# Kernel optimization log

Measured on AMD Instinct MI355X. Metric: run time of the kernel, lower is better.

The kernel has to match this reference:

```python
import jax, jax.numpy as jnp
import numpy as np
import math

L = 12      # n_layer (alternating adaptive True/False)
H = 8       # n_head
C = 256     # n_embd
DH = C // H # head dim = 32
BS = 828    # block_size
T = 827     # seq len after dropping last token
VOCAB = 16384
CAM = 30
IMG = 256


def get_sinusoid(n_position, d_hid):
    pos = np.arange(n_position)[:, None].astype(np.float64)
    hid = np.arange(d_hid)[None, :]
    angle = pos / np.power(10000.0, 2.0 * (hid // 2) / d_hid)
    table = np.zeros_like(angle)
    table[:, 0::2] = np.sin(angle[:, 0::2])
    table[:, 1::2] = np.cos(angle[:, 1::2])
    return jnp.asarray(table[None], jnp.float32)  # [1, n_position, d_hid]


def layer_norm(x, w, b):
    m = x.mean(-1, keepdims=True)
    v = ((x - m) ** 2).mean(-1, keepdims=True)
    return (x - m) * jax.lax.rsqrt(v + 1e-5) * w + b


def setup_inputs() -> dict:
    key = jax.random.key(0)
    ks = iter(jax.random.split(key, 64))
    nrm = lambda shape, s=1.0: jax.random.normal(next(ks), shape, jnp.float32) * s
    B = 4
    inp = {
        'dc_emb': nrm((B, 572, C)),
        'z_emb': nrm((B, 256, C)),
        'p1': nrm((B, CAM)),
        'p2': nrm((B, CAM)),
        'p3': nrm((B, CAM)),
        'frame_emb': nrm((1, 256, C), 0.02),
        'camera_emb': nrm((1, 30, C), 0.02),
        'time_emb': get_sinusoid(BS, C),
        'loc_W1': nrm((2 * CAM, CAM), 0.02), 'loc_b1': jnp.zeros((2 * CAM,)),
        'loc_W2': nrm((IMG * IMG, 2 * CAM), 0.02), 'loc_b2': jnp.zeros((IMG * IMG,)),
        'ln1_w': jnp.ones((L, C)), 'ln1_b': jnp.zeros((L, C)),
        'Wq': nrm((L, C, C), 0.02), 'bq': jnp.zeros((L, C)),
        'Wk': nrm((L, C, C), 0.02), 'bk': jnp.zeros((L, C)),
        'Wv': nrm((L, C, C), 0.02), 'bv': jnp.zeros((L, C)),
        'Wo': nrm((L, C, C), 0.02), 'bo': jnp.zeros((L, C)),
        'ln2_w': jnp.ones((L, C)), 'ln2_b': jnp.zeros((L, C)),
        'W1': nrm((L, 4 * C, C), 0.02), 'b1': jnp.zeros((L, 4 * C)),
        'W2': nrm((L, C, 4 * C), 0.02), 'b2': jnp.zeros((L, C)),
        'lnf_w': jnp.ones((C,)), 'lnf_b': jnp.zeros((C,)),
        'head_W': nrm((VOCAB, C), 0.02),
    }
    return inp


def _forward(dc_emb, z_emb, p1, p2, p3, frame_emb, camera_emb, time_emb,
             loc_W1, loc_b1, loc_W2, loc_b2,
             ln1_w, ln1_b, Wq, bq, Wk, bk, Wv, bv, Wo, bo,
             ln2_w, ln2_b, W1, b1, W2, b2, lnf_w, lnf_b, head_W):
    B = dc_emb.shape[0]
    scale = 1.0 / math.sqrt(DH)

    # AdaptiveAttention bias h: [B, 1, BS, BS] with three 256x256 learned blocks
    def locality(p):
        z = jax.nn.gelu(p @ loc_W1.T + loc_b1, approximate=False)
        z = z @ loc_W2.T + loc_b2
        return z.reshape(B, IMG, IMG)

    h = jnp.zeros((B, 1, BS, BS), dc_emb.dtype)
    h = h.at[:, 0, 285:541, 0:256].set(locality(p1))
    h = h.at[:, 0, 571:827, 0:256].set(locality(p2))
    h = h.at[:, 0, 571:827, 286:542].set(locality(p3))
    h = h[:, :, :T, :T]

    # token + role + time embeddings
    tok = jnp.concatenate([dc_emb, z_emb], axis=1)[:, :-1, :]  # [B, T, C]
    role = jnp.concatenate([frame_emb, camera_emb, frame_emb, camera_emb, frame_emb], axis=1)[:, :T, :]
    x = tok + role + time_emb[:, :T, :]

    causal = jnp.tril(jnp.ones((T, T), bool))  # [T, T]

    for i in range(L):
        adaptive = (i % 2 == 0)
        xn = layer_norm(x, ln1_w[i], ln1_b[i])
        q = (xn @ Wq[i].T + bq[i]).reshape(B, T, H, DH)
        k = (xn @ Wk[i].T + bk[i]).reshape(B, T, H, DH)
        v = (xn @ Wv[i].T + bv[i]).reshape(B, T, H, DH)
        att = jnp.einsum('bqhd,bkhd->bhqk', q, k) * scale
        if adaptive:
            att = att + h
        att = jnp.where(causal, att, -jnp.inf)
        att = jax.nn.softmax(att, axis=-1)
        y = jnp.einsum('bhqk,bkhd->bqhd', att, v).reshape(B, T, C)
        x = x + y @ Wo[i].T + bo[i]
        xn2 = layer_norm(x, ln2_w[i], ln2_b[i])
        x = x + jax.nn.gelu(xn2 @ W1[i].T + b1[i], approximate=False) @ W2[i].T + b2[i]

    x = layer_norm(x, lnf_w, lnf_b)
    logits = x @ head_W.T  # [B, T, VOCAB]
    return logits


def reference(dc_emb, z_emb, p1, p2, p3, frame_emb, camera_emb, time_emb,
              loc_W1, loc_b1, loc_W2, loc_b2,
              ln1_w, ln1_b, Wq, bq, Wk, bk, Wv, bv, Wo, bo,
              ln2_w, ln2_b, W1, b1, W2, b2, lnf_w, lnf_b, head_W):
    return _forward(dc_emb, z_emb, p1, p2, p3, frame_emb, camera_emb, time_emb,
                    loc_W1, loc_b1, loc_W2, loc_b2,
                    ln1_w, ln1_b, Wq, bq, Wk, bk, Wv, bv, Wo, bo,
                    ln2_w, ln2_b, W1, b1, W2, b2, lnf_w, lnf_b, head_W)
```

## Files before the change

kernel.cpp:

```cpp
#include <hip/hip_runtime.h>
#include <hip/hip_bf16.h>
#include <math.h>

#define T_LEN 827
#define M_ROWS 3308
#define NLAYER 12

typedef __attribute__((ext_vector_type(4))) float f32x4;
typedef __attribute__((ext_vector_type(8))) short bf16x8;

__device__ __forceinline__ float gelu_f(float x) {
    return 0.5f * x * (1.0f + erff(x * 0.70710678118654752440f));
}

__device__ __forceinline__ short f2bf_s(float x) {
    __hip_bfloat16 h = __float2bfloat16(x);
    return *reinterpret_cast<short*>(&h);
}

__global__ void cvt_kernel(const float* __restrict__ in, __hip_bfloat16* __restrict__ out, int n4) {
    int i = blockIdx.x * blockDim.x + threadIdx.x;
    if (i >= n4) return;
    float4 v = reinterpret_cast<const float4*>(in)[i];
    out[4*i+0] = __float2bfloat16(v.x);
    out[4*i+1] = __float2bfloat16(v.y);
    out[4*i+2] = __float2bfloat16(v.z);
    out[4*i+3] = __float2bfloat16(v.w);
}

__global__ void prep_wqkv_kernel(const float* __restrict__ Wq, const float* __restrict__ Wk,
                                 const float* __restrict__ Wv, __hip_bfloat16* __restrict__ out) {
    int i = blockIdx.x * 256 + threadIdx.x;
    if (i >= 12*768*64) return;
    int el = i * 4;
    int layer = el / (768*256);
    int rem = el % (768*256);
    int row = rem >> 8, col = rem & 255;
    const float* src;
    float sc = 1.f;
    if (row < 256)      { src = Wq + ((size_t)layer*256 + row)*256 + col; sc = 0.17677669529663687f; }
    else if (row < 512) { src = Wk + ((size_t)layer*256 + (row-256))*256 + col; }
    else                { src = Wv + ((size_t)layer*256 + (row-512))*256 + col; }
    float4 v = *reinterpret_cast<const float4*>(src);
    out[el+0] = __float2bfloat16(v.x * sc);
    out[el+1] = __float2bfloat16(v.y * sc);
    out[el+2] = __float2bfloat16(v.z * sc);
    out[el+3] = __float2bfloat16(v.w * sc);
}

__global__ void prep_bqkv_kernel(const float* __restrict__ bq, const float* __restrict__ bk,
                                 const float* __restrict__ bv, float* __restrict__ out) {
    int i = blockIdx.x * 256 + threadIdx.x;
    if (i >= 12*768) return;
    int layer = i / 768, row = i % 768;
    float v;
    if (row < 256)      v = bq[layer*256 + row] * 0.17677669529663687f;
    else if (row < 512) v = bk[layer*256 + (row-256)];
    else                v = bv[layer*256 + (row-512)];
    out[i] = v;
}

__global__ void zero_kernel(float* __restrict__ p, int n) {
    for (int i = blockIdx.x * blockDim.x + threadIdx.x; i < n; i += gridDim.x * blockDim.x)
        p[i] = 0.f;
}

__global__ void loc_z1_kernel(const float* __restrict__ p1, const float* __restrict__ p2,
                              const float* __restrict__ p3, const float* __restrict__ W1,
                              const float* __restrict__ b1, float* __restrict__ z1) {
    for (int i = threadIdx.x; i < 720; i += 256) {
        int pi = i / 240, rem = i % 240, b = rem / 60, j = rem % 60;
        const float* p = (pi == 0) ? p1 : ((pi == 1) ? p2 : p3);
        float acc = b1[j];
        #pragma unroll
        for (int c = 0; c < 30; ++c) acc += p[b*30 + c] * W1[j*30 + c];
        z1[i] = gelu_f(acc);
    }
}

__global__ void h_fill_kernel(const float* __restrict__ z1, const float* __restrict__ W2,
                              const float* __restrict__ b2, float* __restrict__ h) {
    __shared__ float z[720];
    int tid = threadIdx.x;
    for (int i = tid; i < 720; i += 256) z[i] = z1[i];
    __syncthreads();
    int j = blockIdx.x * 256 + tid;
    float w[60];
    #pragma unroll
    for (int c = 0; c < 60; ++c) w[c] = W2[(size_t)j*60 + c];
    float bj = b2[j];
    int r = j >> 8, cc = j & 255;
    const int br[3] = {285, 571, 571};
    const int bc[3] = {0, 0, 286};
    #pragma unroll
    for (int pi = 0; pi < 3; ++pi) {
        for (int b = 0; b < 4; ++b) {
            float acc = bj;
            #pragma unroll
            for (int c = 0; c < 60; ++c) acc += z[pi*240 + b*60 + c] * w[c];
            h[(size_t)b*T_LEN*T_LEN + (size_t)(br[pi] + r)*T_LEN + bc[pi] + cc] = acc;
        }
    }
}

__global__ void init_x_kernel(const float* __restrict__ dc, const float* __restrict__ z,
                              const float* __restrict__ frame, const float* __restrict__ cam,
                              const float* __restrict__ timeE, float* __restrict__ x) {
    int idx = blockIdx.x * 256 + threadIdx.x;
    int m = idx >> 8, c = idx & 255;
    int b = m / T_LEN, t = m % T_LEN;
    float tok = (t < 572) ? dc[((size_t)b*572 + t)*256 + c]
                          : z[((size_t)b*256 + (t - 572))*256 + c];
    float role;
    if      (t < 256) role = frame[t*256 + c];
    else if (t < 286) role = cam[(t-256)*256 + c];
    else if (t < 542) role = frame[(t-286)*256 + c];
    else if (t < 572) role = cam[(t-542)*256 + c];
    else              role = frame[(t-572)*256 + c];
    x[idx] = tok + role + timeE[t*256 + c];
}

__global__ __launch_bounds__(256) void ln_kernel(const float* __restrict__ x,
                                                 const float* __restrict__ w,
                                                 const float* __restrict__ b,
                                                 __hip_bfloat16* __restrict__ out) {
    int row = blockIdx.x, tid = threadIdx.x;
    float v = x[(size_t)row*256 + tid];
    float s = v;
    #pragma unroll
    for (int off = 32; off; off >>= 1) s += __shfl_down(s, off);
    __shared__ float red[4];
    if ((tid & 63) == 0) red[tid >> 6] = s;
    __syncthreads();
    float mean = (red[0] + red[1] + red[2] + red[3]) * (1.f/256.f);
    float d = v - mean;
    float s2 = d * d;
    #pragma unroll
    for (int off = 32; off; off >>= 1) s2 += __shfl_down(s2, off);
    __shared__ float red2[4];
    if ((tid & 63) == 0) red2[tid >> 6] = s2;
    __syncthreads();
    float var = (red2[0] + red2[1] + red2[2] + red2[3]) * (1.f/256.f);
    float rs = rsqrtf(var + 1e-5f);
    out[(size_t)row*256 + tid] = __float2bfloat16(d * rs * w[tid] + b[tid]);
}

template<int ACT, bool OUTBF16, bool RESID>
__global__ __launch_bounds__(256) void gemm_kernel(const __hip_bfloat16* __restrict__ A,
                                                   const __hip_bfloat16* __restrict__ W,
                                                   const float* __restrict__ bias,
                                                   const float* __restrict__ resid,
                                                   void* __restrict__ out,
                                                   int M, int N, int K, float alpha) {
    __shared__ __hip_bfloat16 As[64][40];
    __shared__ __hip_bfloat16 Bs[64][40];
    const int tid = threadIdx.x;
    const int m0 = blockIdx.x * 64;
    const int n0 = blockIdx.y * 64;
    const int wid = tid >> 6, lane = tid & 63;
    const int wm = wid >> 1, wn = wid & 1;
    const int fr = lane & 15, fq = lane >> 4;
    const int srow = tid >> 2;
    const int scol = (tid & 3) * 8;

    f32x4 acc[2][2];
    #pragma unroll
    for (int mi = 0; mi < 2; ++mi)
        #pragma unroll
        for (int ni = 0; ni < 2; ++ni)
            acc[mi][ni] = (f32x4){0.f, 0.f, 0.f, 0.f};

    for (int k0 = 0; k0 < K; k0 += 32) {
        int gm = m0 + srow;
        uint4 av = make_uint4(0u, 0u, 0u, 0u);
        if (gm < M) av = *reinterpret_cast<const uint4*>(A + (size_t)gm*K + k0 + scol);
        *reinterpret_cast<uint4*>(&As[srow][scol]) = av;
        int gn = n0 + srow;
        uint4 bv = *reinterpret_cast<const uint4*>(W + (size_t)gn*K + k0 + scol);
        *reinterpret_cast<uint4*>(&Bs[srow][scol]) = bv;
        __syncthreads();
        bf16x8 af[2], bfr[2];
        af[0] = *reinterpret_cast<const bf16x8*>(&As[wm*32 + fr][fq*8]);
        af[1] = *reinterpret_cast<const bf16x8*>(&As[wm*32 + 16 + fr][fq*8]);
        bfr[0] = *reinterpret_cast<const bf16x8*>(&Bs[wn*32 + fr][fq*8]);
        bfr[1] = *reinterpret_cast<const bf16x8*>(&Bs[wn*32 + 16 + fr][fq*8]);
        #pragma unroll
        for (int mi = 0; mi < 2; ++mi)
            #pragma unroll
            for (int ni = 0; ni < 2; ++ni)
                acc[mi][ni] = __builtin_amdgcn_mfma_f32_16x16x32_bf16(af[mi], bfr[ni], acc[mi][ni], 0, 0, 0);
        __syncthreads();
    }

    #pragma unroll
    for (int mi = 0; mi < 2; ++mi) {
        #pragma unroll
        for (int ni = 0; ni < 2; ++ni) {
            int n = n0 + wn*32 + ni*16 + fr;
            float bv = bias ? bias[n] : 0.f;
            #pragma unroll
            for (int r = 0; r < 4; ++r) {
                int m = m0 + wm*32 + mi*16 + fq*4 + r;
                if (m >= M) continue;
                float v = (acc[mi][ni][r] + bv) * alpha;
                if (RESID) v += resid[(size_t)m*N + n];
                if (ACT == 1) v = gelu_f(v);
                if (OUTBF16) ((__hip_bfloat16*)out)[(size_t)m*N + n] = __float2bfloat16(v);
                else         ((float*)out)[(size_t)m*N + n] = v;
            }
        }
    }
}

template<int ADAPT>
__global__ __launch_bounds__(256) void attn_mfma_kernel(const __hip_bfloat16* __restrict__ qkv,
                                                        const float* __restrict__ hbuf,
                                                        __hip_bfloat16* __restrict__ y) {
    const int qi = blockIdx.x, hh = blockIdx.y, b = blockIdx.z;
    const int tid = threadIdx.x;
    const int w = tid >> 6, lane = tid & 63;
    const int c = lane & 15, g = lane >> 4;
    const int q0 = qi * 64;
    const int qw0 = q0 + w * 16;

    __shared__ short Ks[64][40];
    __shared__ short Vt[32][72];
    __shared__ short Pw[4][16][72];

    int qrow = qw0 + c; if (qrow > T_LEN-1) qrow = T_LEN-1;
    bf16x8 aq = *reinterpret_cast<const bf16x8*>(qkv + ((size_t)b*T_LEN + qrow)*768 + hh*32 + g*8);

    float m_r[4] = {-INFINITY, -INFINITY, -INFINITY, -INFINITY};
    float l_r[4] = {0.f, 0.f, 0.f, 0.f};
    f32x4 acc[2];
    acc[0] = (f32x4){0.f,0.f,0.f,0.f};
    acc[1] = (f32x4){0.f,0.f,0.f,0.f};

    const int nk = min(q0 + 64, T_LEN);
    const int srow = tid >> 2;
    const int scol8 = (tid & 3) * 8;

    for (int kb = 0; kb < nk; kb += 64) {
        int krow = kb + srow; if (krow > T_LEN-1) krow = T_LEN-1;
        const __hip_bfloat16* kvbase = qkv + ((size_t)b*T_LEN + krow)*768 + hh*32 + scol8;
        bf16x8 kv8 = *reinterpret_cast<const bf16x8*>(kvbase + 256);
        *reinterpret_cast<bf16x8*>(&Ks[srow][scol8]) = kv8;
        bf16x8 vv8 = *reinterpret_cast<const bf16x8*>(kvbase + 512);
        #pragma unroll
        for (int jj = 0; jj < 8; ++jj) Vt[scol8 + jj][srow] = vv8[jj];
        __syncthreads();

        f32x4 sc4[4];
        #pragma unroll
        for (int j = 0; j < 4; ++j) {
            bf16x8 bk = *reinterpret_cast<const bf16x8*>(&Ks[j*16 + c][g*8]);
            sc4[j] = __builtin_amdgcn_mfma_f32_16x16x32_bf16(aq, bk, (f32x4){0.f,0.f,0.f,0.f}, 0, 0, 0);
        }

        float sv[4][4];
        #pragma unroll
        for (int j = 0; j < 4; ++j) {
            int kk = kb + j*16 + c;
            #pragma unroll
            for (int r = 0; r < 4; ++r) {
                int qq = qw0 + g*4 + r;
                bool valid = (qq < T_LEN) && (kk <= qq);
                float s = sc4[j][r];
                if (ADAPT) s += valid ? hbuf[((size_t)b*T_LEN + qq)*T_LEN + kk] : 0.f;
                sv[j][r] = valid ? s : -INFINITY;
            }
        }

        float rm[4], rs[4], sf[4];
        #pragma unroll
        for (int r = 0; r < 4; ++r) {
            float m = fmaxf(fmaxf(sv[0][r], sv[1][r]), fmaxf(sv[2][r], sv[3][r]));
            #pragma unroll
            for (int msk = 1; msk <= 8; msk <<= 1) m = fmaxf(m, __shfl_xor(m, msk));
            float mn = fmaxf(m_r[r], m);
            sf[r] = __expf(m_r[r] - mn);
            m_r[r] = mn;
        }
        float p[4][4];
        #pragma unroll
        for (int r = 0; r < 4; ++r) {
            float su = 0.f;
            #pragma unroll
            for (int j = 0; j < 4; ++j) {
                float e = __expf(sv[j][r] - m_r[r]);
                p[j][r] = e;
                su += e;
            }
            #pragma unroll
            for (int msk = 1; msk <= 8; msk <<= 1) su += __shfl_xor(su, msk);
            rs[r] = su;
            l_r[r] = l_r[r] * sf[r] + rs[r];
            acc[0][r] *= sf[r];
            acc[1][r] *= sf[r];
        }

        #pragma unroll
        for (int j = 0; j < 4; ++j)
            #pragma unroll
            for (int r = 0; r < 4; ++r)
                Pw[w][g*4 + r][j*16 + c] = f2bf_s(p[j][r]);

        #pragma unroll
        for (int kc = 0; kc < 2; ++kc) {
            bf16x8 ap = *reinterpret_cast<const bf16x8*>(&Pw[w][c][kc*32 + g*8]);
            #pragma unroll
            for (int dt = 0; dt < 2; ++dt) {
                bf16x8 bv = *reinterpret_cast<const bf16x8*>(&Vt[dt*16 + c][kc*32 + g*8]);
                acc[dt] = __builtin_amdgcn_mfma_f32_16x16x32_bf16(ap, bv, acc[dt], 0, 0, 0);
            }
        }
        __syncthreads();
    }

    #pragma unroll
    for (int r = 0; r < 4; ++r) {
        int qq = qw0 + g*4 + r;
        if (qq >= T_LEN) continue;
        float inv = 1.f / l_r[r];
        #pragma unroll
        for (int dt = 0; dt < 2; ++dt)
            y[((size_t)b*T_LEN + qq)*256 + hh*32 + dt*16 + c] = __float2bfloat16(acc[dt][r] * inv);
    }
}

extern "C" void kernel_launch(void* const* d_in, const int* in_sizes, int n_in,
                              void* d_out, int out_size, void* d_ws, size_t ws_size,
                              hipStream_t stream) {
    const float* dc    = (const float*)d_in[0];
    const float* zemb  = (const float*)d_in[1];
    const float* p1    = (const float*)d_in[2];
    const float* p2    = (const float*)d_in[3];
    const float* p3    = (const float*)d_in[4];
    const float* frame = (const float*)d_in[5];
    const float* cam   = (const float*)d_in[6];
    const float* timeE = (const float*)d_in[7];
    const float* locW1 = (const float*)d_in[8];
    const float* locb1 = (const float*)d_in[9];
    const float* locW2 = (const float*)d_in[10];
    const float* locb2 = (const float*)d_in[11];
    const float* ln1w  = (const float*)d_in[12];
    const float* ln1b  = (const float*)d_in[13];
    const float* Wq    = (const float*)d_in[14];
    const float* bq    = (const float*)d_in[15];
    const float* Wk    = (const float*)d_in[16];
    const float* bk    = (const float*)d_in[17];
    const float* Wv    = (const float*)d_in[18];
    const float* bv    = (const float*)d_in[19];
    const float* Wo    = (const float*)d_in[20];
    const float* bo    = (const float*)d_in[21];
    const float* ln2w  = (const float*)d_in[22];
    const float* ln2b  = (const float*)d_in[23];
    const float* W1p   = (const float*)d_in[24];
    const float* b1p   = (const float*)d_in[25];
    const float* W2p   = (const float*)d_in[26];
    const float* b2p   = (const float*)d_in[27];
    const float* lnfw  = (const float*)d_in[28];
    const float* lnfb  = (const float*)d_in[29];
    const float* headW = (const float*)d_in[30];

    char* wsb = (char*)d_ws;
    size_t off = 0;
    auto alloc = [&](size_t bytes) -> char* {
        char* p = wsb + off;
        off += (bytes + 255) & ~(size_t)255;
        return p;
    };
    __hip_bfloat16* wqkv_bf = (__hip_bfloat16*)alloc(12ull*768*256*2);
    float*          bqkv    = (float*)alloc(12ull*768*4);
    __hip_bfloat16* wo_bf = (__hip_bfloat16*)alloc(12ull*65536*2);
    __hip_bfloat16* w1_bf = (__hip_bfloat16*)alloc(12ull*262144*2);
    __hip_bfloat16* w2_bf = (__hip_bfloat16*)alloc(12ull*262144*2);
    __hip_bfloat16* wh_bf = (__hip_bfloat16*)alloc(16384ull*256*2);
    float* hbuf = (float*)alloc(4ull*T_LEN*T_LEN*4);
    float* x    = (float*)alloc((size_t)M_ROWS*256*4);
    __hip_bfloat16* xn   = (__hip_bfloat16*)alloc((size_t)M_ROWS*256*2);
    __hip_bfloat16* qkvb = (__hip_bfloat16*)alloc((size_t)M_ROWS*768*2);
    __hip_bfloat16* yb   = (__hip_bfloat16*)alloc((size_t)M_ROWS*256*2);
    __hip_bfloat16* mid  = (__hip_bfloat16*)alloc((size_t)M_ROWS*1024*2);
    float* z1   = (float*)alloc(720*4);

    prep_wqkv_kernel<<<(12*768*64 + 255)/256, 256, 0, stream>>>(Wq, Wk, Wv, wqkv_bf);
    prep_bqkv_kernel<<<36, 256, 0, stream>>>(bq, bk, bv, bqkv);
    cvt_kernel<<<768, 256, 0, stream>>>(Wo, wo_bf, 196608);
    cvt_kernel<<<3072, 256, 0, stream>>>(W1p, w1_bf, 786432);
    cvt_kernel<<<3072, 256, 0, stream>>>(W2p, w2_bf, 786432);
    cvt_kernel<<<4096, 256, 0, stream>>>(headW, wh_bf, 1048576);

    loc_z1_kernel<<<1, 256, 0, stream>>>(p1, p2, p3, locW1, locb1, z1);
    zero_kernel<<<2048, 256, 0, stream>>>(hbuf, 4*T_LEN*T_LEN);
    h_fill_kernel<<<256, 256, 0, stream>>>(z1, locW2, locb2, hbuf);

    init_x_kernel<<<M_ROWS, 256, 0, stream>>>(dc, zemb, frame, cam, timeE, x);

    dim3 g256((M_ROWS + 63)/64, 256/64);
    dim3 g768((M_ROWS + 63)/64, 768/64);
    dim3 g1024((M_ROWS + 63)/64, 1024/64);
    dim3 gattn(13, 8, 4);

    for (int i = 0; i < NLAYER; ++i) {
        ln_kernel<<<M_ROWS, 256, 0, stream>>>(x, ln1w + i*256, ln1b + i*256, xn);
        gemm_kernel<0,true,false><<<g768, 256, 0, stream>>>(xn, wqkv_bf + (size_t)i*768*256, bqkv + i*768, nullptr, qkvb, M_ROWS, 768, 256, 1.f);
        if (i % 2 == 0) attn_mfma_kernel<1><<<gattn, 256, 0, stream>>>(qkvb, hbuf, yb);
        else            attn_mfma_kernel<0><<<gattn, 256, 0, stream>>>(qkvb, hbuf, yb);
        gemm_kernel<0,false,true><<<g256, 256, 0, stream>>>(yb, wo_bf + (size_t)i*65536, bo + i*256, x, x, M_ROWS, 256, 256, 1.f);
        ln_kernel<<<M_ROWS, 256, 0, stream>>>(x, ln2w + i*256, ln2b + i*256, xn);
        gemm_kernel<1,true,false><<<g1024, 256, 0, stream>>>(xn, w1_bf + (size_t)i*262144, b1p + i*1024, nullptr, mid, M_ROWS, 1024, 256, 1.f);
        gemm_kernel<0,false,true><<<g256, 256, 0, stream>>>(mid, w2_bf + (size_t)i*262144, b2p + i*256, x, x, M_ROWS, 256, 1024, 1.f);
    }

    ln_kernel<<<M_ROWS, 256, 0, stream>>>(x, lnfw, lnfb, xn);
    gemm_kernel<0,false,false><<<dim3(52, 256), 256, 0, stream>>>(xn, wh_bf, nullptr, nullptr, (float*)d_out, M_ROWS, 16384, 256, 1.f);
}
```

Before: 1.173 ms.

## Fuse layernorms into GEMMs, fuse MLP, and double-buffer attention K/V

Replaces the generic K-looped GEMM with a K=256 single-shot kernel that optionally applies layernorm on the A-operand load. It fuses LN2+FC1+GELU+FC2+residual (and the final LN) into one MLP kernel that keeps the hidden activations in shared memory. The attention kernel double-buffers K/V tiles with register prefetch and drops one barrier per iteration. This removes the separate LN launches and the 1024-wide intermediate round-trip through global memory. In exchange, the MLP kernel launches only 104 blocks and reads weights directly from global memory, which may leave the GPU underoccupied.

```diff
diff --git a/kernel.cpp b/kernel.cpp
--- a/kernel.cpp
+++ b/kernel.cpp
@@ -120,49 +120,68 @@
     x[idx] = tok + role + timeE[t*256 + c];
 }
 
-__global__ __launch_bounds__(256) void ln_kernel(const float* __restrict__ x,
-                                                 const float* __restrict__ w,
-                                                 const float* __restrict__ b,
-                                                 __hip_bfloat16* __restrict__ out) {
-    int row = blockIdx.x, tid = threadIdx.x;
-    float v = x[(size_t)row*256 + tid];
-    float s = v;
-    #pragma unroll
-    for (int off = 32; off; off >>= 1) s += __shfl_down(s, off);
-    __shared__ float red[4];
-    if ((tid & 63) == 0) red[tid >> 6] = s;
+template<bool LN, bool RESID, bool OUTBF16>
+__global__ __launch_bounds__(256) void gemm_k256(
+    const float* __restrict__ xsrc, const float* __restrict__ lnw, const float* __restrict__ lnb,
+    const __hip_bfloat16* __restrict__ Abf,
+    const __hip_bfloat16* __restrict__ W, const float* __restrict__ bias,
+    const float* __restrict__ resid, void* __restrict__ out, int M, int N)
+{
+    __shared__ __hip_bfloat16 As[64][264];
+    __shared__ __hip_bfloat16 Bs[64][264];
+    __shared__ float redS[4][64], redQ[4][64];
+    const int tid = threadIdx.x;
+    const int m0 = blockIdx.x * 64, n0 = blockIdx.y * 64;
+    const int r = tid >> 2, sg = tid & 3;
+
+    {
+        const __hip_bfloat16* bsrc = W + (size_t)(n0 + r) * 256 + sg * 8;
+        #pragma unroll
+        for (int j = 0; j < 8; ++j)
+            *reinterpret_cast<uint4*>(&Bs[r][sg*8 + j*32]) =
+                *reinterpret_cast<const uint4*>(bsrc + j*32);
+    }
+    int gr = m0 + r; if (gr > M-1) gr = M-1;
+    if constexpr (LN) {
+        const float* src = xsrc + (size_t)gr * 256;
+        float s = 0.f, q = 0.f;
+        #pragma unroll
+        for (int j = 0; j < 8; ++j) {
+            int k = sg*8 + j*32;
+            float4 a = *reinterpret_cast<const float4*>(src + k);
+            float4 c4 = *reinterpret_cast<const float4*>(src + k + 4);
+            s += a.x + a.y + a.z + a.w + c4.x + c4.y + c4.z + c4.w;
+            q += a.x*a.x + a.y*a.y + a.z*a.z + a.w*a.w
+               + c4.x*c4.x + c4.y*c4.y + c4.z*c4.z + c4.w*c4.w;
+        }
+        redS[sg][r] = s; redQ[sg][r] = q;
+        __syncthreads();
+        float mean = (redS[0][r] + redS[1][r] + redS[2][r] + redS[3][r]) * (1.f/256.f);
+        float msq  = (redQ[0][r] + redQ[1][r] + redQ[2][r] + redQ[3][r]) * (1.f/256.f);
+        float rstd = rsqrtf(msq - mean*mean + 1e-5f);
+        #pragma unroll
+        for (int j = 0; j < 8; ++j) {
+            int k = sg*8 + j*32;
+            float4 a = *reinterpret_cast<const float4*>(src + k);
+            float4 c4 = *reinterpret_cast<const float4*>(src + k + 4);
+            float v[8] = {a.x, a.y, a.z, a.w, c4.x, c4.y, c4.z, c4.w};
+            bf16x8 pk;
+            #pragma unroll
+            for (int e = 0; e < 8; ++e)
+                pk[e] = f2bf_s((v[e] - mean) * rstd * lnw[k+e] + lnb[k+e]);
+            *reinterpret_cast<bf16x8*>(&As[r][k]) = pk;
+        }
+    } else {
+        const __hip_bfloat16* asrc = Abf + (size_t)gr * 256 + sg * 8;
+        #pragma unroll
+        for (int j = 0; j < 8; ++j)
+            *reinterpret_cast<uint4*>(&As[r][sg*8 + j*32]) =
+                *reinterpret_cast<const uint4*>(asrc + j*32);
+    }
     __syncthreads();
-    float mean = (red[0] + red[1] + red[2] + red[3]) * (1.f/256.f);
-    float d = v - mean;
-    float s2 = d * d;
-    #pragma unroll
-    for (int off = 32; off; off >>= 1) s2 += __shfl_down(s2, off);
-    __shared__ float red2[4];
-    if ((tid & 63) == 0) red2[tid >> 6] = s2;
-    __syncthreads();
-    float var = (red2[0] + red2[1] + red2[2] + red2[3]) * (1.f/256.f);
-    float rs = rsqrtf(var + 1e-5f);
-    out[(size_t)row*256 + tid] = __float2bfloat16(d * rs * w[tid] + b[tid]);
-}
-
-template<int ACT, bool OUTBF16, bool RESID>
-__global__ __launch_bounds__(256) void gemm_kernel(const __hip_bfloat16* __restrict__ A,
-                                                   const __hip_bfloat16* __restrict__ W,
-                                                   const float* __restrict__ bias,
-                                                   const float* __restrict__ resid,
-                                                   void* __restrict__ out,
-                                                   int M, int N, int K, float alpha) {
-    __shared__ __hip_bfloat16 As[64][40];
-    __shared__ __hip_bfloat16 Bs[64][40];
-    const int tid = threadIdx.x;
-    const int m0 = blockIdx.x * 64;
-    const int n0 = blockIdx.y * 64;
+
     const int wid = tid >> 6, lane = tid & 63;
-    const int wm = wid >> 1, wn = wid & 1;
-    const int fr = lane & 15, fq = lane >> 4;
-    const int srow = tid >> 2;
-    const int scol = (tid & 3) * 8;
-
+    const int wm = wid >> 1, wn = wid & 1, c = lane & 15, g = lane >> 4;
     f32x4 acc[2][2];
     #pragma unroll
     for (int mi = 0; mi < 2; ++mi)
@@ -170,44 +189,170 @@
         for (int ni = 0; ni < 2; ++ni)
             acc[mi][ni] = (f32x4){0.f, 0.f, 0.f, 0.f};
 
-    for (int k0 = 0; k0 < K; k0 += 32) {
-        int gm = m0 + srow;
-        uint4 av = make_uint4(0u, 0u, 0u, 0u);
-        if (gm < M) av = *reinterpret_cast<const uint4*>(A + (size_t)gm*K + k0 + scol);
-        *reinterpret_cast<uint4*>(&As[srow][scol]) = av;
-        int gn = n0 + srow;
-        uint4 bv = *reinterpret_cast<const uint4*>(W + (size_t)gn*K + k0 + scol);
-        *reinterpret_cast<uint4*>(&Bs[srow][scol]) = bv;
-        __syncthreads();
-        bf16x8 af[2], bfr[2];
-        af[0] = *reinterpret_cast<const bf16x8*>(&As[wm*32 + fr][fq*8]);
-        af[1] = *reinterpret_cast<const bf16x8*>(&As[wm*32 + 16 + fr][fq*8]);
-        bfr[0] = *reinterpret_cast<const bf16x8*>(&Bs[wn*32 + fr][fq*8]);
-        bfr[1] = *reinterpret_cast<const bf16x8*>(&Bs[wn*32 + 16 + fr][fq*8]);
-        #pragma unroll
-        for (int mi = 0; mi < 2; ++mi)
-            #pragma unroll
-            for (int ni = 0; ni < 2; ++ni)
-                acc[mi][ni] = __builtin_amdgcn_mfma_f32_16x16x32_bf16(af[mi], bfr[ni], acc[mi][ni], 0, 0, 0);
-        __syncthreads();
+    #pragma unroll
+    for (int kj = 0; kj < 8; ++kj) {
+        bf16x8 a0 = *reinterpret_cast<const bf16x8*>(&As[wm*32 + c][kj*32 + g*8]);
+        bf16x8 a1 = *reinterpret_cast<const bf16x8*>(&As[wm*32 + 16 + c][kj*32 + g*8]);
+        bf16x8 b0 = *reinterpret_cast<const bf16x8*>(&Bs[wn*32 + c][kj*32 + g*8]);
+        bf16x8 b1v = *reinterpret_cast<const bf16x8*>(&Bs[wn*32 + 16 + c][kj*32 + g*8]);
+        acc[0][0] = __builtin_amdgcn_mfma_f32_16x16x32_bf16(a0, b0, acc[0][0], 0, 0, 0);
+        acc[0][1] = __builtin_amdgcn_mfma_f32_16x16x32_bf16(a0, b1v, acc[0][1], 0, 0, 0);
+        acc[1][0] = __builtin_amdgcn_mfma_f32_16x16x32_bf16(a1, b0, acc[1][0], 0, 0, 0);
+        acc[1][1] = __builtin_amdgcn_mfma_f32_16x16x32_bf16(a1, b1v, acc[1][1], 0, 0, 0);
     }
 
     #pragma unroll
     for (int mi = 0; mi < 2; ++mi) {
         #pragma unroll
         for (int ni = 0; ni < 2; ++ni) {
-            int n = n0 + wn*32 + ni*16 + fr;
-            float bv = bias ? bias[n] : 0.f;
-            #pragma unroll
-            for (int r = 0; r < 4; ++r) {
-                int m = m0 + wm*32 + mi*16 + fq*4 + r;
+            int n = n0 + wn*32 + ni*16 + c;
+            float bb = bias ? bias[n] : 0.f;
+            #pragma unroll
+            for (int rg = 0; rg < 4; ++rg) {
+                int m = m0 + wm*32 + mi*16 + g*4 + rg;
                 if (m >= M) continue;
-                float v = (acc[mi][ni][r] + bv) * alpha;
+                float v = acc[mi][ni][rg] + bb;
                 if (RESID) v += resid[(size_t)m*N + n];
-                if (ACT == 1) v = gelu_f(v);
                 if (OUTBF16) ((__hip_bfloat16*)out)[(size_t)m*N + n] = __float2bfloat16(v);
                 else         ((float*)out)[(size_t)m*N + n] = v;
             }
+        }
+    }
+}
+
+template<bool FINAL>
+__global__ __launch_bounds__(512) void mlp_fused(
+    float* __restrict__ x,
+    const float* __restrict__ ln2w, const float* __restrict__ ln2b,
+    const __hip_bfloat16* __restrict__ W1, const float* __restrict__ b1,
+    const __hip_bfloat16* __restrict__ W2, const float* __restrict__ b2,
+    const float* __restrict__ lnfw, const float* __restrict__ lnfb,
+    __hip_bfloat16* __restrict__ xn)
+{
+    __shared__ __hip_bfloat16 As[32][264];
+    __shared__ __hip_bfloat16 Ms[32][1044];
+    const int tid = threadIdx.x;
+    const int m0 = blockIdx.x * 32;
+    const int w = tid >> 6, lane = tid & 63, c = lane & 15, g = lane >> 4;
+
+    {
+        int r = tid >> 4, p = tid & 15;
+        int gr = m0 + r; if (gr > M_ROWS-1) gr = M_ROWS-1;
+        const float* src = x + (size_t)gr*256 + p*16;
+        float4 f0 = *reinterpret_cast<const float4*>(src);
+        float4 f1 = *reinterpret_cast<const float4*>(src + 4);
+        float4 f2 = *reinterpret_cast<const float4*>(src + 8);
+        float4 f3 = *reinterpret_cast<const float4*>(src + 12);
+        float vv[16] = {f0.x,f0.y,f0.z,f0.w, f1.x,f1.y,f1.z,f1.w,
+                        f2.x,f2.y,f2.z,f2.w, f3.x,f3.y,f3.z,f3.w};
+        float s = 0.f, q = 0.f;
+        #pragma unroll
+        for (int e = 0; e < 16; ++e) { s += vv[e]; q += vv[e]*vv[e]; }
+        #pragma unroll
+        for (int msk = 1; msk <= 8; msk <<= 1) { s += __shfl_xor(s, msk); q += __shfl_xor(q, msk); }
+        float mean = s * (1.f/256.f);
+        float rstd = rsqrtf(q*(1.f/256.f) - mean*mean + 1e-5f);
+        bf16x8 pk0, pk1;
+        #pragma unroll
+        for (int e = 0; e < 8; ++e) {
+            pk0[e] = f2bf_s((vv[e]   - mean)*rstd*ln2w[p*16+e]   + ln2b[p*16+e]);
+            pk1[e] = f2bf_s((vv[8+e] - mean)*rstd*ln2w[p*16+8+e] + ln2b[p*16+8+e]);
+        }
+        *reinterpret_cast<bf16x8*>(&As[r][p*16])     = pk0;
+        *reinterpret_cast<bf16x8*>(&As[r][p*16 + 8]) = pk1;
+    }
+    __syncthreads();
+
+    #pragma unroll 1
+    for (int ns = 0; ns < 8; ++ns) {
+        int nb = w*128 + ns*16;
+        const __hip_bfloat16* wrow = W1 + (size_t)(nb + c)*256 + g*8;
+        f32x4 a0 = (f32x4){0.f,0.f,0.f,0.f}, a1 = (f32x4){0.f,0.f,0.f,0.f};
+        #pragma unroll
+        for (int kj = 0; kj < 8; ++kj) {
+            bf16x8 bfrag = *reinterpret_cast<const bf16x8*>(wrow + kj*32);
+            bf16x8 af0 = *reinterpret_cast<const bf16x8*>(&As[c][kj*32 + g*8]);
+            bf16x8 af1 = *reinterpret_cast<const bf16x8*>(&As[16 + c][kj*32 + g*8]);
+            a0 = __builtin_amdgcn_mfma_f32_16x16x32_bf16(af0, bfrag, a0, 0, 0, 0);
+            a1 = __builtin_amdgcn_mfma_f32_16x16x32_bf16(af1, bfrag, a1, 0, 0, 0);
+        }
+        float bb = b1[nb + c];
+        #pragma unroll
+        for (int rg = 0; rg < 4; ++rg) {
+            Ms[g*4 + rg][nb + c]      = __float2bfloat16(gelu_f(a0[rg] + bb));
+            Ms[16 + g*4 + rg][nb + c] = __float2bfloat16(gelu_f(a1[rg] + bb));
+        }
+    }
+    __syncthreads();
+
+    f32x4 o[2][2];
+    #pragma unroll
+    for (int i = 0; i < 2; ++i)
+        #pragma unroll
+        for (int j = 0; j < 2; ++j)
+            o[i][j] = (f32x4){0.f,0.f,0.f,0.f};
+    #pragma unroll
+    for (int ns2 = 0; ns2 < 2; ++ns2) {
+        int nb = w*32 + ns2*16;
+        const __hip_bfloat16* wrow = W2 + (size_t)(nb + c)*1024 + g*8;
+        #pragma unroll
+        for (int kj = 0; kj < 32; ++kj) {
+            bf16x8 bfrag = *reinterpret_cast<const bf16x8*>(wrow + kj*32);
+            bf16x8 af0 = *reinterpret_cast<const bf16x8*>(&Ms[c][kj*32 + g*8]);
+            bf16x8 af1 = *reinterpret_cast<const bf16x8*>(&Ms[16 + c][kj*32 + g*8]);
+            o[ns2][0] = __builtin_amdgcn_mfma_f32_16x16x32_bf16(af0, bfrag, o[ns2][0], 0, 0, 0);
+            o[ns2][1] = __builtin_amdgcn_mfma_f32_16x16x32_bf16(af1, bfrag, o[ns2][1], 0, 0, 0);
+        }
+    }
+    __syncthreads();
+
+    float* xf = reinterpret_cast<float*>(&Ms[0][0]);
+    #pragma unroll
+    for (int ns2 = 0; ns2 < 2; ++ns2) {
+        int nb = w*32 + ns2*16;
+        float bb = b2[nb + c];
+        #pragma unroll
+        for (int mi = 0; mi < 2; ++mi) {
+            #pragma unroll
+            for (int rg = 0; rg < 4; ++rg) {
+                int row = mi*16 + g*4 + rg;
+                int gm = m0 + row;
+                if (gm < M_ROWS) {
+                    float v = o[ns2][mi][rg] + bb + x[(size_t)gm*256 + nb + c];
+                    x[(size_t)gm*256 + nb + c] = v;
+                    if (FINAL) xf[row*256 + nb + c] = v;
+                }
+            }
+        }
+    }
+
+    if constexpr (FINAL) {
+        __syncthreads();
+        int r = tid >> 4, p = tid & 15;
+        int gm = m0 + r;
+        const float* src = xf + r*256 + p*16;
+        float4 f0 = *reinterpret_cast<const float4*>(src);
+        float4 f1 = *reinterpret_cast<const float4*>(src + 4);
+        float4 f2 = *reinterpret_cast<const float4*>(src + 8);
+        float4 f3 = *reinterpret_cast<const float4*>(src + 12);
+        float vv[16] = {f0.x,f0.y,f0.z,f0.w, f1.x,f1.y,f1.z,f1.w,
+                        f2.x,f2.y,f2.z,f2.w, f3.x,f3.y,f3.z,f3.w};
+        float s = 0.f, q = 0.f;
+        #pragma unroll
+        for (int e = 0; e < 16; ++e) { s += vv[e]; q += vv[e]*vv[e]; }
+        #pragma unroll
+        for (int msk = 1; msk <= 8; msk <<= 1) { s += __shfl_xor(s, msk); q += __shfl_xor(q, msk); }
+        float mean = s * (1.f/256.f);
+        float rstd = rsqrtf(q*(1.f/256.f) - mean*mean + 1e-5f);
+        if (gm < M_ROWS) {
+            bf16x8 pk0, pk1;
+            #pragma unroll
+            for (int e = 0; e < 8; ++e) {
+                pk0[e] = f2bf_s((vv[e]   - mean)*rstd*lnfw[p*16+e]   + lnfb[p*16+e]);
+                pk1[e] = f2bf_s((vv[8+e] - mean)*rstd*lnfw[p*16+8+e] + lnfb[p*16+8+e]);
+            }
+            *reinterpret_cast<bf16x8*>(&xn[(size_t)gm*256 + p*16])     = pk0;
+            *reinterpret_cast<bf16x8*>(&xn[(size_t)gm*256 + p*16 + 8]) = pk1;
         }
     }
 }
@@ -223,8 +368,8 @@
     const int q0 = qi * 64;
     const int qw0 = q0 + w * 16;
 
-    __shared__ short Ks[64][40];
-    __shared__ short Vt[32][72];
+    __shared__ short Ks[2][64][40];
+    __shared__ short Vt[2][32][68];
     __shared__ short Pw[4][16][72];
 
     int qrow = qw0 + c; if (qrow > T_LEN-1) qrow = T_LEN-1;
@@ -237,23 +382,36 @@
     acc[1] = (f32x4){0.f,0.f,0.f,0.f};
 
     const int nk = min(q0 + 64, T_LEN);
+    const int nit = (nk + 63) >> 6;
     const int srow = tid >> 2;
     const int scol8 = (tid & 3) * 8;
 
-    for (int kb = 0; kb < nk; kb += 64) {
-        int krow = kb + srow; if (krow > T_LEN-1) krow = T_LEN-1;
-        const __hip_bfloat16* kvbase = qkv + ((size_t)b*T_LEN + krow)*768 + hh*32 + scol8;
-        bf16x8 kv8 = *reinterpret_cast<const bf16x8*>(kvbase + 256);
-        *reinterpret_cast<bf16x8*>(&Ks[srow][scol8]) = kv8;
-        bf16x8 vv8 = *reinterpret_cast<const bf16x8*>(kvbase + 512);
-        #pragma unroll
-        for (int jj = 0; jj < 8; ++jj) Vt[scol8 + jj][srow] = vv8[jj];
+    bf16x8 kreg, vreg;
+    {
+        int krow = srow; if (krow > T_LEN-1) krow = T_LEN-1;
+        const __hip_bfloat16* base = qkv + ((size_t)b*T_LEN + krow)*768 + hh*32 + scol8;
+        kreg = *reinterpret_cast<const bf16x8*>(base + 256);
+        vreg = *reinterpret_cast<const bf16x8*>(base + 512);
+    }
+
+    for (int it = 0; it < nit; ++it) {
+        const int bsel = it & 1;
+        const int kb = it * 64;
+        *reinterpret_cast<bf16x8*>(&Ks[bsel][srow][scol8]) = kreg;
+        #pragma unroll
+        for (int jj = 0; jj < 8; ++jj) Vt[bsel][scol8 + jj][srow] = vreg[jj];
         __syncthreads();
+        if (it + 1 < nit) {
+            int krow = kb + 64 + srow; if (krow > T_LEN-1) krow = T_LEN-1;
+            const __hip_bfloat16* base = qkv + ((size_t)b*T_LEN + krow)*768 + hh*32 + scol8;
+            kreg = *reinterpret_cast<const bf16x8*>(base + 256);
+            vreg = *reinterpret_cast<const bf16x8*>(base + 512);
+        }
 
         f32x4 sc4[4];
         #pragma unroll
         for (int j = 0; j < 4; ++j) {
-            bf16x8 bk = *reinterpret_cast<const bf16x8*>(&Ks[j*16 + c][g*8]);
+            bf16x8 bk = *reinterpret_cast<const bf16x8*>(&Ks[bsel][j*16 + c][g*8]);
             sc4[j] = __builtin_amdgcn_mfma_f32_16x16x32_bf16(aq, bk, (f32x4){0.f,0.f,0.f,0.f}, 0, 0, 0);
         }
 
@@ -262,69 +420,67 @@
         for (int j = 0; j < 4; ++j) {
             int kk = kb + j*16 + c;
             #pragma unroll
-            for (int r = 0; r < 4; ++r) {
-                int qq = qw0 + g*4 + r;
+            for (int rg = 0; rg < 4; ++rg) {
+                int qq = qw0 + g*4 + rg;
                 bool valid = (qq < T_LEN) && (kk <= qq);
-                float s = sc4[j][r];
+                float s = sc4[j][rg];
                 if (ADAPT) s += valid ? hbuf[((size_t)b*T_LEN + qq)*T_LEN + kk] : 0.f;
-                sv[j][r] = valid ? s : -INFINITY;
+                sv[j][rg] = valid ? s : -INFINITY;
             }
         }
 
-        float rm[4], rs[4], sf[4];
-        #pragma unroll
-        for (int r = 0; r < 4; ++r) {
-            float m = fmaxf(fmaxf(sv[0][r], sv[1][r]), fmaxf(sv[2][r], sv[3][r]));
+        float sf[4];
+        #pragma unroll
+        for (int rg = 0; rg < 4; ++rg) {
+            float m = fmaxf(fmaxf(sv[0][rg], sv[1][rg]), fmaxf(sv[2][rg], sv[3][rg]));
             #pragma unroll
             for (int msk = 1; msk <= 8; msk <<= 1) m = fmaxf(m, __shfl_xor(m, msk));
-            float mn = fmaxf(m_r[r], m);
-            sf[r] = __expf(m_r[r] - mn);
-            m_r[r] = mn;
+            float mn = fmaxf(m_r[rg], m);
+            sf[rg] = __expf(m_r[rg] - mn);
+            m_r[rg] = mn;
         }
         float p[4][4];
         #pragma unroll
-        for (int r = 0; r < 4; ++r) {
+        for (int rg = 0; rg < 4; ++rg) {
             float su = 0.f;
             #pragma unroll
             for (int j = 0; j < 4; ++j) {
-                float e = __expf(sv[j][r] - m_r[r]);
-                p[j][r] = e;
+                float e = __expf(sv[j][rg] - m_r[rg]);
+                p[j][rg] = e;
                 su += e;
             }
             #pragma unroll
             for (int msk = 1; msk <= 8; msk <<= 1) su += __shfl_xor(su, msk);
-            rs[r] = su;
-            l_r[r] = l_r[r] * sf[r] + rs[r];
-            acc[0][r] *= sf[r];
-            acc[1][r] *= sf[r];
+            l_r[rg] = l_r[rg] * sf[rg] + su;
+            acc[0][rg] *= sf[rg];
+            acc[1][rg] *= sf[rg];
         }
 
         #pragma unroll
         for (int j = 0; j < 4; ++j)
             #pragma unroll
-            for (int r = 0; r < 4; ++r)
-                Pw[w][g*4 + r][j*16 + c] = f2bf_s(p[j][r]);
+            for (int rg = 0; rg < 4; ++rg)
+                Pw[w][g*4 + rg][j*16 + c] = f2bf_s(p[j][rg]);
 
         #pragma unroll
         for (int kc = 0; kc < 2; ++kc) {
             bf16x8 ap = *reinterpret_cast<const bf16x8*>(&Pw[w][c][kc*32 + g*8]);
             #pragma unroll
             for (int dt = 0; dt < 2; ++dt) {
-                bf16x8 bv = *reinterpret_cast<const bf16x8*>(&Vt[dt*16 + c][kc*32 + g*8]);
+                bf16x8 bv = *reinterpret_cast<const bf16x8*>(&Vt[bsel][dt*16 + c][kc*32 + g*8]);
                 acc[dt] = __builtin_amdgcn_mfma_f32_16x16x32_bf16(ap, bv, acc[dt], 0, 0, 0);
             }
         }
-        __syncthreads();
-    }
-
-    #pragma unroll
-    for (int r = 0; r < 4; ++r) {
-        int qq = qw0 + g*4 + r;
+    }
+
+    #pragma unroll
+    for (int rg = 0; rg < 4; ++rg) {
+        int qq = qw0 + g*4 + rg;
         if (qq >= T_LEN) continue;
-        float inv = 1.f / l_r[r];
+        float inv = 1.f / l_r[rg];
         #pragma unroll
         for (int dt = 0; dt < 2; ++dt)
-            y[((size_t)b*T_LEN + qq)*256 + hh*32 + dt*16 + c] = __float2bfloat16(acc[dt][r] * inv);
+            y[((size_t)b*T_LEN + qq)*256 + hh*32 + dt*16 + c] = __float2bfloat16(acc[dt][rg] * inv);
     }
 }
 
@@ -381,7 +537,6 @@
     __hip_bfloat16* xn   = (__hip_bfloat16*)alloc((size_t)M_ROWS*256*2);
     __hip_bfloat16* qkvb = (__hip_bfloat16*)alloc((size_t)M_ROWS*768*2);
     __hip_bfloat16* yb   = (__hip_bfloat16*)alloc((size_t)M_ROWS*256*2);
-    __hip_bfloat16* mid  = (__hip_bfloat16*)alloc((size_t)M_ROWS*1024*2);
     float* z1   = (float*)alloc(720*4);
 
     prep_wqkv_kernel<<<(12*768*64 + 255)/256, 256, 0, stream>>>(Wq, Wk, Wv, wqkv_bf);
@@ -397,22 +552,31 @@
 
     init_x_kernel<<<M_ROWS, 256, 0, stream>>>(dc, zemb, frame, cam, timeE, x);
 
-    dim3 g256((M_ROWS + 63)/64, 256/64);
-    dim3 g768((M_ROWS + 63)/64, 768/64);
-    dim3 g1024((M_ROWS + 63)/64, 1024/64);
+    dim3 gqkv(52, 12);
+    dim3 goproj(52, 4);
     dim3 gattn(13, 8, 4);
 
     for (int i = 0; i < NLAYER; ++i) {
-        ln_kernel<<<M_ROWS, 256, 0, stream>>>(x, ln1w + i*256, ln1b + i*256, xn);
-        gemm_kernel<0,true,false><<<g768, 256, 0, stream>>>(xn, wqkv_bf + (size_t)i*768*256, bqkv + i*768, nullptr, qkvb, M_ROWS, 768, 256, 1.f);
+        gemm_k256<true,false,true><<<gqkv, 256, 0, stream>>>(
+            x, ln1w + i*256, ln1b + i*256, nullptr,
+            wqkv_bf + (size_t)i*196608, bqkv + i*768, nullptr, qkvb, M_ROWS, 768);
         if (i % 2 == 0) attn_mfma_kernel<1><<<gattn, 256, 0, stream>>>(qkvb, hbuf, yb);
         else            attn_mfma_kernel<0><<<gattn, 256, 0, stream>>>(qkvb, hbuf, yb);
-        gemm_kernel<0,false,true><<<g256, 256, 0, stream>>>(yb, wo_bf + (size_t)i*65536, bo + i*256, x, x, M_ROWS, 256, 256, 1.f);
-        ln_kernel<<<M_ROWS, 256, 0, stream>>>(x, ln2w + i*256, ln2b + i*256, xn);
-        gemm_kernel<1,true,false><<<g1024, 256, 0, stream>>>(xn, w1_bf + (size_t)i*262144, b1p + i*1024, nullptr, mid, M_ROWS, 1024, 256, 1.f);
-        gemm_kernel<0,false,true><<<g256, 256, 0, stream>>>(mid, w2_bf + (size_t)i*262144, b2p + i*256, x, x, M_ROWS, 256, 1024, 1.f);
-    }
-
-    ln_kernel<<<M_ROWS, 256, 0, stream>>>(x, lnfw, lnfb, xn);
-    gemm_kernel<0,false,false><<<dim3(52, 256), 256, 0, stream>>>(xn, wh_bf, nullptr, nullptr, (float*)d_out, M_ROWS, 16384, 256, 1.f);
-}
+        gemm_k256<false,true,false><<<goproj, 256, 0, stream>>>(
+            nullptr, nullptr, nullptr, yb,
+            wo_bf + (size_t)i*65536, bo + i*256, x, x, M_ROWS, 256);
+        if (i == NLAYER-1)
+            mlp_fused<true><<<104, 512, 0, stream>>>(
+                x, ln2w + i*256, ln2b + i*256,
+                w1_bf + (size_t)i*262144, b1p + i*1024,
+                w2_bf + (size_t)i*262144, b2p + i*256, lnfw, lnfb, xn);
+        else
+            mlp_fused<false><<<104, 512, 0, stream>>>(
+                x, ln2w + i*256, ln2b + i*256,
+                w1_bf + (size_t)i*262144, b1p + i*1024,
+                w2_bf + (size_t)i*262144, b2p + i*256, nullptr, nullptr, nullptr);
+    }
+
+    gemm_k256<false,false,false><<<dim3(52, 256), 256, 0, stream>>>(
+        nullptr, nullptr, nullptr, xn, wh_bf, nullptr, nullptr, (float*)d_out, M_ROWS, 16384);
+}
```

Measured after the change: 1.183 ms. No clear change (+0.8%).
